# Performance work log

Measured on AMD Instinct MI355X. Metric: run time of the kernel, lower is better.

Reference implementation:

```python
import jax, jax.numpy as jnp
import numpy as np

B, L, E, DC, N = 1024, 64, 1024, 768, 16384
EPS = 1e-08


def setup_inputs() -> dict:
    key = jax.random.key(0)
    k1, k2, k3, k4, k5, k6 = jax.random.split(key, 6)
    inputs = jax.random.normal(k1, (B, 1, E), dtype=jnp.float32)
    text_emb = jax.random.normal(k2, (B, L, DC), dtype=jnp.float32)
    # padding mask: True = padded; valid lengths in [10, 60) so every row triggers the insert branch
    lengths = jax.random.randint(k3, (B,), 10, 60)
    attn_mask = jnp.arange(L)[None, :] >= lengths[:, None]
    proj_w = jax.random.normal(k4, (DC, E), dtype=jnp.float32) * 0.02
    proj_b = jnp.zeros((DC,), dtype=jnp.float32)
    codebook = jax.random.normal(k5, (N, DC), dtype=jnp.float32) * 0.02
    return {"inputs": inputs, "text_emb": text_emb, "attn_mask": attn_mask,
            "proj_w": proj_w, "proj_b": proj_b, "codebook": codebook}


def _soft_match(x, W):
    # x: [B, S, D], W: [N, D] -> soft codebook readout [B, S, D]
    xn = x / jnp.maximum(jnp.linalg.norm(x, axis=-1, keepdims=True), EPS)
    Wn = W / jnp.maximum(jnp.linalg.norm(W, axis=-1, keepdims=True), EPS)
    d = 1.0 - jnp.einsum('bsd,nd->bsn', xn, Wn)   # 1 - cosine similarity
    p = jax.nn.softmax(d, axis=-1)                 # softmax over codebook entries
    return jnp.einsum('bsn,nd->bsd', p, W)


def reference(inputs, text_emb, attn_mask, proj_w, proj_b, codebook):
    # proj: torch Linear -> x @ W.T + b
    x = jnp.einsum('bse,de->bsd', inputs, proj_w) + proj_b
    clue = _soft_match(x, codebook)                # [B, 1, DC]

    b, l = attn_mask.shape
    vl = l - jnp.sum(attn_mask, axis=1)            # valid length per row, [B]
    do = vl < 64                                   # insert only if there is room
    pos = jnp.arange(l)
    at_vl = pos[None, :] == vl[:, None]            # position valid_length
    at_prev = pos[None, :] == (vl - 1)[:, None]    # position valid_length-1
    prev_vec = text_emb[jnp.arange(b), jnp.clip(vl - 1, 0, l - 1)]  # [B, DC]

    sel_vl = (do[:, None] & at_vl)[..., None]
    sel_prev = (do[:, None] & at_prev)[..., None]
    new_text_emb = jnp.where(sel_vl, prev_vec[:, None, :], text_emb)
    new_text_emb = jnp.where(sel_prev, clue[:, 0, :][:, None, :], new_text_emb)
    new_attn_mask = attn_mask & ~(do[:, None] & at_vl)
    return new_text_emb, new_attn_mask, jnp.float32(0.0)
```

## Files before the change

kernel.cpp:

```cpp
#include <hip/hip_runtime.h>
#include <hip/hip_bf16.h>

#define B_  1024
#define L_  64
#define E_  1024
#define DC_ 768
#define N_  16384
#define NZ_ 16

typedef short bf16x8 __attribute__((ext_vector_type(8)));
typedef float f32x4  __attribute__((ext_vector_type(4)));


__global__ void detect_mask(const unsigned int* __restrict__ mi, int* __restrict__ flag) {
    __shared__ int notInt, notFlt;
    if (threadIdx.x == 0) { notInt = 0; notFlt = 0; }
    __syncthreads();
    int ni = 0, nf = 0;
    for (int i = threadIdx.x; i < 16384; i += 256) {
        unsigned v = mi[i];
        if (v > 1u) ni = 1;
        if (v != 0u && v != 0x3f800000u) nf = 1;
    }
    if (ni) notInt = 1;
    if (nf) notFlt = 1;
    __syncthreads();
    if (threadIdx.x == 0) *flag = (!notInt) ? 1 : ((!notFlt) ? 2 : 0);
}

__global__ void compute_vl(const void* __restrict__ mask, const int* __restrict__ flag,
                           int* __restrict__ vl) {
    int b = blockIdx.x * blockDim.x + threadIdx.x;
    if (b >= B_) return;
    int f = *flag;
    int s = 0;
    if (f == 1) {
        const int* m = (const int*)mask;
        for (int j = 0; j < L_; ++j) s += m[b * L_ + j];
    } else if (f == 2) {
        const float* m = (const float*)mask;
        for (int j = 0; j < L_; ++j) s += (m[b * L_ + j] != 0.0f) ? 1 : 0;
    } else {
        const unsigned char* m = (const unsigned char*)mask;
        for (int j = 0; j < L_; ++j) s += m[b * L_ + j];
    }
    vl[b] = L_ - s;
}

__global__ __launch_bounds__(256) void rownorm(const float* __restrict__ M,
                                               float* __restrict__ r, int cols) {
    int row = blockIdx.x;
    const float* p = M + (size_t)row * cols;
    float s = 0.0f;
    for (int c = threadIdx.x; c < cols; c += 256) { float v = p[c]; s += v * v; }
    for (int off = 32; off > 0; off >>= 1) s += __shfl_down(s, off);
    __shared__ float sm[4];
    if ((threadIdx.x & 63) == 0) sm[threadIdx.x >> 6] = s;
    __syncthreads();
    if (threadIdx.x == 0) {
        float t = sm[0] + sm[1] + sm[2] + sm[3];
        r[row] = 1.0f / fmaxf(sqrtf(t), 1e-8f);
    }
}

__global__ __launch_bounds__(256) void rownorm_bf16(const __hip_bfloat16* __restrict__ M,
                                                    float* __restrict__ r, int cols) {
    int row = blockIdx.x;
    const __hip_bfloat16* p = M + (size_t)row * cols;
    float s = 0.0f;
    for (int c = threadIdx.x; c < cols; c += 256) { float v = __bfloat162float(p[c]); s += v * v; }
    for (int off = 32; off > 0; off >>= 1) s += __shfl_down(s, off);
    __shared__ float sm[4];
    if ((threadIdx.x & 63) == 0) sm[threadIdx.x >> 6] = s;
    __syncthreads();
    if (threadIdx.x == 0) {
        float t = sm[0] + sm[1] + sm[2] + sm[3];
        r[row] = 1.0f / fmaxf(sqrtf(t), 1e-8f);
    }
}

__global__ __launch_bounds__(256) void prep_cb(const float* __restrict__ CB,
                                               __hip_bfloat16* __restrict__ CBb,
                                               __hip_bfloat16* __restrict__ CBt) {
    __shared__ float t[64][65];
    int n0 = blockIdx.x * 64, d0 = blockIdx.y * 64;
    int tid = threadIdx.x;
    #pragma unroll
    for (int i = 0; i < 16; ++i) {
        int r = (tid >> 6) + i * 4, c = tid & 63;
        float v = CB[(size_t)(n0 + r) * DC_ + d0 + c];
        t[r][c] = v;
        CBb[(size_t)(n0 + r) * DC_ + d0 + c] = __float2bfloat16(v);
    }
    __syncthreads();
    #pragma unroll
    for (int i = 0; i < 16; ++i) {
        int r = (tid >> 6) + i * 4, c = tid & 63;
        CBt[(size_t)(d0 + r) * N_ + n0 + c] = __float2bfloat16(t[c][r]);
    }
}

__global__ __launch_bounds__(256) void cast_bf16(const float* __restrict__ src,
                                                 ushort* __restrict__ dst, int n4) {
    int idx = blockIdx.x * 256 + threadIdx.x;
    if (idx >= n4) return;
    float4 v = ((const float4*)src)[idx];
    ushort4 o;
    __hip_bfloat16 h0 = __float2bfloat16(v.x); o.x = __builtin_bit_cast(ushort, h0);
    __hip_bfloat16 h1 = __float2bfloat16(v.y); o.y = __builtin_bit_cast(ushort, h1);
    __hip_bfloat16 h2 = __float2bfloat16(v.z); o.z = __builtin_bit_cast(ushort, h2);
    __hip_bfloat16 h3 = __float2bfloat16(v.w); o.w = __builtin_bit_cast(ushort, h3);
    ((ushort4*)dst)[idx] = o;
}

__device__ __forceinline__ void stage_tile(const __hip_bfloat16* __restrict__ src, size_t ldk,
                                           __hip_bfloat16* smem, int wave, int lane) {
    #pragma unroll
    for (int s = 0; s < 2; ++s) {
        const int chunk = wave * 32 + s * 16;
        const int r = chunk + (lane >> 2);
        const int gslot = (lane & 3) ^ ((lane >> 2) & 3);
        const __hip_bfloat16* g = src + (size_t)r * ldk + gslot * 8;
        __builtin_amdgcn_global_load_lds(
            (const __attribute__((address_space(1))) void*)g,
            (__attribute__((address_space(3))) void*)(smem + chunk * 32), 16, 0, 0);
    }
}

__device__ __forceinline__ bf16x8 read_frag(const __hip_bfloat16* smem, int base_row, int lane) {
    const int r = base_row + (lane & 15);
    const int slot = ((lane >> 4) ^ r) & 3;
    return *(const bf16x8*)(smem + r * 32 + slot * 8);
}

__global__ __launch_bounds__(256) void proj_mfma(const __hip_bfloat16* __restrict__ inb,
                                                 const __hip_bfloat16* __restrict__ pwb,
                                                 const float* __restrict__ bias,
                                                 __hip_bfloat16* __restrict__ Xb) {
    __shared__ __align__(16) __hip_bfloat16 As[128 * 32];
    __shared__ __align__(16) __hip_bfloat16 Bs[128 * 32];
    const int t = threadIdx.x, lane = t & 63, wave = t >> 6;
    const int wr = wave >> 1, wc = wave & 1;
    const int m0 = blockIdx.y * 128, n0 = blockIdx.x * 128;

    f32x4 acc[4][4];
    #pragma unroll
    for (int i = 0; i < 4; ++i)
        #pragma unroll
        for (int j = 0; j < 4; ++j) acc[i][j] = (f32x4){0.f, 0.f, 0.f, 0.f};

    const __hip_bfloat16* Asrc = inb + (size_t)m0 * E_;
    const __hip_bfloat16* Bsrc = pwb + (size_t)n0 * E_;
    for (int k0 = 0; k0 < E_; k0 += 32) {
        stage_tile(Asrc + k0, E_, As, wave, lane);
        stage_tile(Bsrc + k0, E_, Bs, wave, lane);
        __syncthreads();
        bf16x8 af[4], bg[4];
        #pragma unroll
        for (int i = 0; i < 4; ++i) af[i] = read_frag(As, wr * 64 + i * 16, lane);
        #pragma unroll
        for (int j = 0; j < 4; ++j) bg[j] = read_frag(Bs, wc * 64 + j * 16, lane);
        #pragma unroll
        for (int i = 0; i < 4; ++i)
            #pragma unroll
            for (int j = 0; j < 4; ++j)
                acc[i][j] = __builtin_amdgcn_mfma_f32_16x16x32_bf16(af[i], bg[j], acc[i][j], 0, 0, 0);
        __syncthreads();
    }

    const int fr = lane & 15, fq = lane >> 4;
    #pragma unroll
    for (int i = 0; i < 4; ++i) {
        const int mb = m0 + wr * 64 + i * 16 + fq * 4;
        #pragma unroll
        for (int j = 0; j < 4; ++j) {
            const int d = n0 + wc * 64 + j * 16 + fr;
            const float bv = bias[d];
            #pragma unroll
            for (int q = 0; q < 4; ++q)
                Xb[(size_t)(mb + q) * DC_ + d] = __float2bfloat16(acc[i][j][q] + bv);
        }
    }
}

__global__ __launch_bounds__(256) void score_mfma(const __hip_bfloat16* __restrict__ Xb,
                                                  const __hip_bfloat16* __restrict__ CBb,
                                                  const float* __restrict__ rX,
                                                  const float* __restrict__ rW,
                                                  __hip_bfloat16* __restrict__ P,
                                                  float* __restrict__ Z) {
    __shared__ __align__(16) __hip_bfloat16 As[128 * 32];
    __shared__ __align__(16) __hip_bfloat16 Bs[128 * 32];
    const int t = threadIdx.x, lane = t & 63, wave = t >> 6;
    const int wr = wave >> 1, wc = wave & 1;
    const int m0 = blockIdx.y * 128, n0 = blockIdx.x * 128;

    f32x4 acc[4][4];
    #pragma unroll
    for (int i = 0; i < 4; ++i)
        #pragma unroll
        for (int j = 0; j < 4; ++j) acc[i][j] = (f32x4){0.f, 0.f, 0.f, 0.f};

    const __hip_bfloat16* Asrc = Xb  + (size_t)m0 * DC_;
    const __hip_bfloat16* Bsrc = CBb + (size_t)n0 * DC_;
    for (int k0 = 0; k0 < DC_; k0 += 32) {
        stage_tile(Asrc + k0, DC_, As, wave, lane);
        stage_tile(Bsrc + k0, DC_, Bs, wave, lane);
        __syncthreads();
        bf16x8 af[4], bg[4];
        #pragma unroll
        for (int i = 0; i < 4; ++i) af[i] = read_frag(As, wr * 64 + i * 16, lane);
        #pragma unroll
        for (int j = 0; j < 4; ++j) bg[j] = read_frag(Bs, wc * 64 + j * 16, lane);
        #pragma unroll
        for (int i = 0; i < 4; ++i)
            #pragma unroll
            for (int j = 0; j < 4; ++j)
                acc[i][j] = __builtin_amdgcn_mfma_f32_16x16x32_bf16(af[i], bg[j], acc[i][j], 0, 0, 0);
        __syncthreads();
    }

    const int fr = lane & 15, fq = lane >> 4;
    float rw[4];
    #pragma unroll
    for (int j = 0; j < 4; ++j) rw[j] = rW[n0 + wc * 64 + j * 16 + fr];
    #pragma unroll
    for (int i = 0; i < 4; ++i) {
        const int mb = m0 + wr * 64 + i * 16 + fq * 4;
        float rx[4];
        #pragma unroll
        for (int q = 0; q < 4; ++q) rx[q] = rX[mb + q];
        float rs[4] = {0.f, 0.f, 0.f, 0.f};
        #pragma unroll
        for (int j = 0; j < 4; ++j) {
            const int n = n0 + wc * 64 + j * 16 + fr;
            #pragma unroll
            for (int q = 0; q < 4; ++q) {
                float e = __expf(-acc[i][j][q] * rx[q] * rw[j]);
                P[(size_t)(mb + q) * N_ + n] = __float2bfloat16(e);
                rs[q] += e;
            }
        }
        #pragma unroll
        for (int q = 0; q < 4; ++q) {
            float s = rs[q];
            s += __shfl_xor(s, 1); s += __shfl_xor(s, 2);
            s += __shfl_xor(s, 4); s += __shfl_xor(s, 8);
            if (fr == 0) atomicAdd(&Z[mb + q], s);
        }
    }
}

__global__ __launch_bounds__(256) void out_mfma(const __hip_bfloat16* __restrict__ P,
                                                const __hip_bfloat16* __restrict__ CBt,
                                                float* __restrict__ cluePart) {
    __shared__ __align__(16) __hip_bfloat16 As[128 * 32];
    __shared__ __align__(16) __hip_bfloat16 Bs[128 * 32];
    const int t = threadIdx.x, lane = t & 63, wave = t >> 6;
    const int wr = wave >> 1, wc = wave & 1;
    const int m0 = blockIdx.y * 128, d0 = blockIdx.x * 128;
    const int kbeg = blockIdx.z * (N_ / NZ_);
    float* outp = cluePart + (size_t)blockIdx.z * (B_ * DC_);

    f32x4 acc[4][4];
    #pragma unroll
    for (int i = 0; i < 4; ++i)
        #pragma unroll
        for (int j = 0; j < 4; ++j) acc[i][j] = (f32x4){0.f, 0.f, 0.f, 0.f};

    const __hip_bfloat16* Asrc = P   + (size_t)m0 * N_;
    const __hip_bfloat16* Bsrc = CBt + (size_t)d0 * N_;
    for (int kk = 0; kk < N_ / NZ_; kk += 32) {
        const int k0 = kbeg + kk;
        stage_tile(Asrc + k0, N_, As, wave, lane);
        stage_tile(Bsrc + k0, N_, Bs, wave, lane);
        __syncthreads();
        bf16x8 af[4], bg[4];
        #pragma unroll
        for (int i = 0; i < 4; ++i) af[i] = read_frag(As, wr * 64 + i * 16, lane);
        #pragma unroll
        for (int j = 0; j < 4; ++j) bg[j] = read_frag(Bs, wc * 64 + j * 16, lane);
        #pragma unroll
        for (int i = 0; i < 4; ++i)
            #pragma unroll
            for (int j = 0; j < 4; ++j)
                acc[i][j] = __builtin_amdgcn_mfma_f32_16x16x32_bf16(af[i], bg[j], acc[i][j], 0, 0, 0);
        __syncthreads();
    }

    const int fr = lane & 15, fq = lane >> 4;
    #pragma unroll
    for (int i = 0; i < 4; ++i) {
        const int mb = m0 + wr * 64 + i * 16 + fq * 4;
        #pragma unroll
        for (int j = 0; j < 4; ++j) {
            const int d = d0 + wc * 64 + j * 16 + fr;
            #pragma unroll
            for (int q = 0; q < 4; ++q)
                outp[(size_t)(mb + q) * DC_ + d] = acc[i][j][q];
        }
    }
}

__global__ __launch_bounds__(256) void reduce_clue(const float* __restrict__ cluePart,
                                                   const float* __restrict__ Z,
                                                   float* __restrict__ clueF) {
    const int d = blockIdx.x * 256 + threadIdx.x;
    const int b = blockIdx.y;
    float s = 0.0f;
    #pragma unroll
    for (int z = 0; z < NZ_; ++z)
        s += cluePart[(size_t)z * (B_ * DC_) + (size_t)b * DC_ + d];
    clueF[(size_t)b * DC_ + d] = s / Z[b];
}

__global__ __launch_bounds__(256) void assemble(const float* __restrict__ text,
                                                const float* __restrict__ clueF,
                                                const int* __restrict__ vl,
                                                float* __restrict__ out) {
    int idx = blockIdx.x * 256 + threadIdx.x;
    int c = idx % 192;
    int bl = idx / 192;
    int l = bl & 63, b = bl >> 6;
    int v = vl[b];
    float4 val;
    if (l == v) {
        val = ((const float4*)text)[(size_t)(b * 64 + v - 1) * 192 + c];
    } else if (l == v - 1) {
        val = ((const float4*)(clueF + (size_t)b * DC_))[c];
    } else {
        val = ((const float4*)text)[idx];
    }
    ((float4*)out)[idx] = val;
}

__global__ void mask_scalar(const int* __restrict__ vl, float* __restrict__ out_mask,
                            float* __restrict__ out_scalar) {
    int idx = blockIdx.x * blockDim.x + threadIdx.x;
    if (idx < B_ * L_) {
        int b = idx >> 6, j = idx & 63;
        out_mask[idx] = (j > vl[b]) ? 1.0f : 0.0f;
    }
    if (idx == 0) *out_scalar = 0.0f;
}

extern "C" void kernel_launch(void* const* d_in, const int* in_sizes, int n_in,
                              void* d_out, int out_size, void* d_ws, size_t ws_size,
                              hipStream_t stream) {
    const float* inputs  = (const float*)d_in[0];
    const float* text    = (const float*)d_in[1];
    const void*  mask    = d_in[2];
    const float* proj_w  = (const float*)d_in[3];
    const float* proj_b  = (const float*)d_in[4];
    const float* codebook= (const float*)d_in[5];
    float* out = (float*)d_out;

    char* ws = (char*)d_ws;
    __hip_bfloat16* Xb       = (__hip_bfloat16*)(ws + 0);
    __hip_bfloat16* CBb      = (__hip_bfloat16*)(ws + 1572864);
    __hip_bfloat16* CBt      = (__hip_bfloat16*)(ws + 26738688);
    __hip_bfloat16* P        = (__hip_bfloat16*)(ws + 51904512);
    __hip_bfloat16* inb      = (__hip_bfloat16*)(ws + 51904512);
    __hip_bfloat16* pwb      = (__hip_bfloat16*)(ws + 54001664);
    float*          cluePart = (float*)(ws + 85458944);
    float*          clueF    = (float*)(ws + 135790592);
    float*          rX       = (float*)(ws + 138936320);
    float*          rW       = (float*)(ws + 138940416);
    float*          Z        = (float*)(ws + 139005952);
    int*            vl       = (int*)(ws + 139010048);
    int*            flag     = (int*)(ws + 139014144);

    hipMemsetAsync(Z, 0, B_ * sizeof(float), stream);

    detect_mask<<<1, 256, 0, stream>>>((const unsigned int*)mask, flag);
    compute_vl<<<4, 256, 0, stream>>>(mask, flag, vl);
    rownorm<<<N_, 256, 0, stream>>>(codebook, rW, DC_);
    prep_cb<<<dim3(N_ / 64, DC_ / 64), 256, 0, stream>>>(codebook, CBb, CBt);
    cast_bf16<<<(B_ * E_ / 4 + 255) / 256, 256, 0, stream>>>(inputs, (ushort*)inb, B_ * E_ / 4);
    cast_bf16<<<(DC_ * E_ / 4 + 255) / 256, 256, 0, stream>>>(proj_w, (ushort*)pwb, DC_ * E_ / 4);
    proj_mfma<<<dim3(DC_ / 128, B_ / 128), 256, 0, stream>>>(inb, pwb, proj_b, Xb);
    rownorm_bf16<<<B_, 256, 0, stream>>>(Xb, rX, DC_);
    score_mfma<<<dim3(N_ / 128, B_ / 128), 256, 0, stream>>>(Xb, CBb, rX, rW, P, Z);
    out_mfma<<<dim3(DC_ / 128, B_ / 128, NZ_), 256, 0, stream>>>(P, CBt, cluePart);
    reduce_clue<<<dim3(DC_ / 256, B_), 256, 0, stream>>>(cluePart, Z, clueF);
    assemble<<<49152, 256, 0, stream>>>(text, clueF, vl, out);
    mask_scalar<<<(B_ * L_ + 255) / 256, 256, 0, stream>>>(
        vl, out + (size_t)B_ * L_ * DC_, out + (size_t)B_ * L_ * DC_ + B_ * L_);
}
```

Before: 594.8 us.

## Switch score and output GEMMs to 32x32x16 MFMA with K=64 swizzled LDS tiles

Replaces the 16x16x32 MFMA tiling in the score and output GEMMs with 32x32x16 MFMA instructions. K-tiles are now 64 wide and staged into LDS with an XOR-swizzled layout through direct global-to-LDS loads. This halves the number of barrier pairs and lowers LDS fragment reads per MFMA. The output GEMM grid is transposed so consecutive blocks share the same codebook columns, which should improve cache reuse. Epilogue indexing is rewritten for the 32x32 accumulator layout, so any mismatch with the hardware lane mapping would produce wrong results.

```diff
diff --git a/kernel.cpp b/kernel.cpp
--- a/kernel.cpp
+++ b/kernel.cpp
@@ -10,6 +10,7 @@
 
 typedef short bf16x8 __attribute__((ext_vector_type(8)));
 typedef float f32x4  __attribute__((ext_vector_type(4)));
+typedef float f32x16 __attribute__((ext_vector_type(16)));
 
 
 __global__ void detect_mask(const unsigned int* __restrict__ mi, int* __restrict__ flag) {
@@ -183,70 +184,96 @@
     }
 }
 
+__device__ __forceinline__ void stage64(const __hip_bfloat16* __restrict__ src, size_t ldk,
+                                        __hip_bfloat16* smem, int wave, int lane) {
+    #pragma unroll
+    for (int s = 0; s < 4; ++s) {
+        const int rowbase = wave * 32 + s * 8;
+        const int r = rowbase + (lane >> 3);
+        const int gslot = (lane & 7) ^ ((lane >> 3) & 7);
+        const __hip_bfloat16* g = src + (size_t)r * ldk + gslot * 8;
+        __builtin_amdgcn_global_load_lds(
+            (const __attribute__((address_space(1))) void*)g,
+            (__attribute__((address_space(3))) void*)(smem + rowbase * 64), 16, 0, 0);
+    }
+}
+
+__device__ __forceinline__ bf16x8 read_frag32(const __hip_bfloat16* smem, int base_row,
+                                              int khalf, int lane) {
+    const int r = base_row + (lane & 31);
+    const int slot = (khalf * 2 + (lane >> 5)) ^ (r & 7);
+    return *(const bf16x8*)(smem + r * 64 + slot * 8);
+}
+
 __global__ __launch_bounds__(256) void score_mfma(const __hip_bfloat16* __restrict__ Xb,
                                                   const __hip_bfloat16* __restrict__ CBb,
                                                   const float* __restrict__ rX,
                                                   const float* __restrict__ rW,
                                                   __hip_bfloat16* __restrict__ P,
                                                   float* __restrict__ Z) {
-    __shared__ __align__(16) __hip_bfloat16 As[128 * 32];
-    __shared__ __align__(16) __hip_bfloat16 Bs[128 * 32];
+    __shared__ __align__(16) __hip_bfloat16 As[128 * 64];
+    __shared__ __align__(16) __hip_bfloat16 Bs[128 * 64];
     const int t = threadIdx.x, lane = t & 63, wave = t >> 6;
     const int wr = wave >> 1, wc = wave & 1;
     const int m0 = blockIdx.y * 128, n0 = blockIdx.x * 128;
 
-    f32x4 acc[4][4];
-    #pragma unroll
-    for (int i = 0; i < 4; ++i)
-        #pragma unroll
-        for (int j = 0; j < 4; ++j) acc[i][j] = (f32x4){0.f, 0.f, 0.f, 0.f};
+    f32x16 acc[2][2];
+    #pragma unroll
+    for (int i = 0; i < 2; ++i)
+        #pragma unroll
+        for (int j = 0; j < 2; ++j) acc[i][j] = (f32x16)(0.f);
 
     const __hip_bfloat16* Asrc = Xb  + (size_t)m0 * DC_;
     const __hip_bfloat16* Bsrc = CBb + (size_t)n0 * DC_;
-    for (int k0 = 0; k0 < DC_; k0 += 32) {
-        stage_tile(Asrc + k0, DC_, As, wave, lane);
-        stage_tile(Bsrc + k0, DC_, Bs, wave, lane);
-        __syncthreads();
-        bf16x8 af[4], bg[4];
-        #pragma unroll
-        for (int i = 0; i < 4; ++i) af[i] = read_frag(As, wr * 64 + i * 16, lane);
-        #pragma unroll
-        for (int j = 0; j < 4; ++j) bg[j] = read_frag(Bs, wc * 64 + j * 16, lane);
-        #pragma unroll
-        for (int i = 0; i < 4; ++i)
+    for (int k0 = 0; k0 < DC_; k0 += 64) {
+        stage64(Asrc + k0, DC_, As, wave, lane);
+        stage64(Bsrc + k0, DC_, Bs, wave, lane);
+        __syncthreads();
+        #pragma unroll
+        for (int h = 0; h < 4; ++h) {
+            bf16x8 a0 = read_frag32(As, wr * 64,      h, lane);
+            bf16x8 a1 = read_frag32(As, wr * 64 + 32, h, lane);
+            bf16x8 b0 = read_frag32(Bs, wc * 64,      h, lane);
+            bf16x8 b1 = read_frag32(Bs, wc * 64 + 32, h, lane);
+            acc[0][0] = __builtin_amdgcn_mfma_f32_32x32x16_bf16(a0, b0, acc[0][0], 0, 0, 0);
+            acc[0][1] = __builtin_amdgcn_mfma_f32_32x32x16_bf16(a0, b1, acc[0][1], 0, 0, 0);
+            acc[1][0] = __builtin_amdgcn_mfma_f32_32x32x16_bf16(a1, b0, acc[1][0], 0, 0, 0);
+            acc[1][1] = __builtin_amdgcn_mfma_f32_32x32x16_bf16(a1, b1, acc[1][1], 0, 0, 0);
+        }
+        __syncthreads();
+    }
+
+    const int col = lane & 31, hi = lane >> 5;
+    float rwj[2];
+    #pragma unroll
+    for (int j = 0; j < 2; ++j) rwj[j] = rW[n0 + wc * 64 + j * 32 + col];
+    #pragma unroll
+    for (int i = 0; i < 2; ++i) {
+        float rs[16];
+        #pragma unroll
+        for (int r = 0; r < 16; ++r) rs[r] = 0.f;
+        #pragma unroll
+        for (int r = 0; r < 16; ++r) {
+            const int m = m0 + wr * 64 + i * 32 + (r & 3) + 8 * (r >> 2) + 4 * hi;
+            const float rx = rX[m];
             #pragma unroll
-            for (int j = 0; j < 4; ++j)
-                acc[i][j] = __builtin_amdgcn_mfma_f32_16x16x32_bf16(af[i], bg[j], acc[i][j], 0, 0, 0);
-        __syncthreads();
-    }
-
-    const int fr = lane & 15, fq = lane >> 4;
-    float rw[4];
-    #pragma unroll
-    for (int j = 0; j < 4; ++j) rw[j] = rW[n0 + wc * 64 + j * 16 + fr];
-    #pragma unroll
-    for (int i = 0; i < 4; ++i) {
-        const int mb = m0 + wr * 64 + i * 16 + fq * 4;
-        float rx[4];
-        #pragma unroll
-        for (int q = 0; q < 4; ++q) rx[q] = rX[mb + q];
-        float rs[4] = {0.f, 0.f, 0.f, 0.f};
-        #pragma unroll
-        for (int j = 0; j < 4; ++j) {
-            const int n = n0 + wc * 64 + j * 16 + fr;
-            #pragma unroll
-            for (int q = 0; q < 4; ++q) {
-                float e = __expf(-acc[i][j][q] * rx[q] * rw[j]);
-                P[(size_t)(mb + q) * N_ + n] = __float2bfloat16(e);
-                rs[q] += e;
+            for (int j = 0; j < 2; ++j) {
+                const int n = n0 + wc * 64 + j * 32 + col;
+                float e = __expf(-acc[i][j][r] * rx * rwj[j]);
+                P[(size_t)m * N_ + n] = __float2bfloat16(e);
+                rs[r] += e;
             }
         }
         #pragma unroll
-        for (int q = 0; q < 4; ++q) {
-            float s = rs[q];
-            s += __shfl_xor(s, 1); s += __shfl_xor(s, 2);
-            s += __shfl_xor(s, 4); s += __shfl_xor(s, 8);
-            if (fr == 0) atomicAdd(&Z[mb + q], s);
+        for (int r = 0; r < 16; ++r) {
+            float s = rs[r];
+            s += __shfl_xor(s, 1);  s += __shfl_xor(s, 2);
+            s += __shfl_xor(s, 4);  s += __shfl_xor(s, 8);
+            s += __shfl_xor(s, 16);
+            if (col == 0) {
+                const int m = m0 + wr * 64 + i * 32 + (r & 3) + 8 * (r >> 2) + 4 * hi;
+                atomicAdd(&Z[m], s);
+            }
         }
     }
 }
@@ -254,52 +281,53 @@
 __global__ __launch_bounds__(256) void out_mfma(const __hip_bfloat16* __restrict__ P,
                                                 const __hip_bfloat16* __restrict__ CBt,
                                                 float* __restrict__ cluePart) {
-    __shared__ __align__(16) __hip_bfloat16 As[128 * 32];
-    __shared__ __align__(16) __hip_bfloat16 Bs[128 * 32];
+    __shared__ __align__(16) __hip_bfloat16 As[128 * 64];
+    __shared__ __align__(16) __hip_bfloat16 Bs[128 * 64];
     const int t = threadIdx.x, lane = t & 63, wave = t >> 6;
     const int wr = wave >> 1, wc = wave & 1;
-    const int m0 = blockIdx.y * 128, d0 = blockIdx.x * 128;
+    const int m0 = blockIdx.x * 128, d0 = blockIdx.y * 128;
     const int kbeg = blockIdx.z * (N_ / NZ_);
     float* outp = cluePart + (size_t)blockIdx.z * (B_ * DC_);
 
-    f32x4 acc[4][4];
-    #pragma unroll
-    for (int i = 0; i < 4; ++i)
-        #pragma unroll
-        for (int j = 0; j < 4; ++j) acc[i][j] = (f32x4){0.f, 0.f, 0.f, 0.f};
+    f32x16 acc[2][2];
+    #pragma unroll
+    for (int i = 0; i < 2; ++i)
+        #pragma unroll
+        for (int j = 0; j < 2; ++j) acc[i][j] = (f32x16)(0.f);
 
     const __hip_bfloat16* Asrc = P   + (size_t)m0 * N_;
     const __hip_bfloat16* Bsrc = CBt + (size_t)d0 * N_;
-    for (int kk = 0; kk < N_ / NZ_; kk += 32) {
+    for (int kk = 0; kk < N_ / NZ_; kk += 64) {
         const int k0 = kbeg + kk;
-        stage_tile(Asrc + k0, N_, As, wave, lane);
-        stage_tile(Bsrc + k0, N_, Bs, wave, lane);
-        __syncthreads();
-        bf16x8 af[4], bg[4];
-        #pragma unroll
-        for (int i = 0; i < 4; ++i) af[i] = read_frag(As, wr * 64 + i * 16, lane);
-        #pragma unroll
-        for (int j = 0; j < 4; ++j) bg[j] = read_frag(Bs, wc * 64 + j * 16, lane);
-        #pragma unroll
-        for (int i = 0; i < 4; ++i)
+        stage64(Asrc + k0, N_, As, wave, lane);
+        stage64(Bsrc + k0, N_, Bs, wave, lane);
+        __syncthreads();
+        #pragma unroll
+        for (int h = 0; h < 4; ++h) {
+            bf16x8 a0 = read_frag32(As, wr * 64,      h, lane);
+            bf16x8 a1 = read_frag32(As, wr * 64 + 32, h, lane);
+            bf16x8 b0 = read_frag32(Bs, wc * 64,      h, lane);
+            bf16x8 b1 = read_frag32(Bs, wc * 64 + 32, h, lane);
+            acc[0][0] = __builtin_amdgcn_mfma_f32_32x32x16_bf16(a0, b0, acc[0][0], 0, 0, 0);
+            acc[0][1] = __builtin_amdgcn_mfma_f32_32x32x16_bf16(a0, b1, acc[0][1], 0, 0, 0);
+            acc[1][0] = __builtin_amdgcn_mfma_f32_32x32x16_bf16(a1, b0, acc[1][0], 0, 0, 0);
+            acc[1][1] = __builtin_amdgcn_mfma_f32_32x32x16_bf16(a1, b1, acc[1][1], 0, 0, 0);
+        }
+        __syncthreads();
+    }
+
+    const int col = lane & 31, hi = lane >> 5;
+    #pragma unroll
+    for (int i = 0; i < 2; ++i)
+        #pragma unroll
+        for (int r = 0; r < 16; ++r) {
+            const int m = m0 + wr * 64 + i * 32 + (r & 3) + 8 * (r >> 2) + 4 * hi;
             #pragma unroll
-            for (int j = 0; j < 4; ++j)
-                acc[i][j] = __builtin_amdgcn_mfma_f32_16x16x32_bf16(af[i], bg[j], acc[i][j], 0, 0, 0);
-        __syncthreads();
-    }
-
-    const int fr = lane & 15, fq = lane >> 4;
-    #pragma unroll
-    for (int i = 0; i < 4; ++i) {
-        const int mb = m0 + wr * 64 + i * 16 + fq * 4;
-        #pragma unroll
-        for (int j = 0; j < 4; ++j) {
-            const int d = d0 + wc * 64 + j * 16 + fr;
-            #pragma unroll
-            for (int q = 0; q < 4; ++q)
-                outp[(size_t)(mb + q) * DC_ + d] = acc[i][j][q];
-        }
-    }
+            for (int j = 0; j < 2; ++j) {
+                const int d = d0 + wc * 64 + j * 32 + col;
+                outp[(size_t)m * DC_ + d] = acc[i][j][r];
+            }
+        }
 }
 
 __global__ __launch_bounds__(256) void reduce_clue(const float* __restrict__ cluePart,
@@ -381,7 +409,7 @@
     proj_mfma<<<dim3(DC_ / 128, B_ / 128), 256, 0, stream>>>(inb, pwb, proj_b, Xb);
     rownorm_bf16<<<B_, 256, 0, stream>>>(Xb, rX, DC_);
     score_mfma<<<dim3(N_ / 128, B_ / 128), 256, 0, stream>>>(Xb, CBb, rX, rW, P, Z);
-    out_mfma<<<dim3(DC_ / 128, B_ / 128, NZ_), 256, 0, stream>>>(P, CBt, cluePart);
+    out_mfma<<<dim3(B_ / 128, DC_ / 128, NZ_), 256, 0, stream>>>(P, CBt, cluePart);
     reduce_clue<<<dim3(DC_ / 256, B_), 256, 0, stream>>>(cluePart, Z, clueF);
     assemble<<<49152, 256, 0, stream>>>(text, clueF, vl, out);
     mask_scalar<<<(B_ * L_ + 255) / 256, 256, 0, stream>>>(
```

Result: slower. 625.4 us (+5.2%).
